# Kernel tuning notes

Measured on AMD Instinct MI355X. Metric: run time of the kernel, lower is better.

The kernel has to match this reference:

```python
import jax, jax.numpy as jnp
import numpy as np

N_INP = 1024
N_HID = 1024
N_OUT = 1024
B, S = 8, 2048


def setup_inputs() -> dict:
    key = jax.random.key(0)
    ks = jax.random.split(key, 9)
    s_in = 1.0 / np.sqrt(N_INP)
    s_hid = 1.0 / np.sqrt(N_HID)
    return {
        "x": jax.random.normal(ks[0], (B, S, N_INP), jnp.float32),
        "wq": jax.random.uniform(ks[1], (N_INP, N_HID), jnp.float32, -s_in, s_in),
        "bq": jax.random.uniform(ks[2], (N_HID,), jnp.float32, -s_in, s_in),
        "wk": jax.random.uniform(ks[3], (N_INP, N_HID), jnp.float32, -s_in, s_in),
        "bk": jax.random.uniform(ks[4], (N_HID,), jnp.float32, -s_in, s_in),
        "wv": jax.random.uniform(ks[5], (N_INP, N_HID), jnp.float32, -s_in, s_in),
        "bv": jax.random.uniform(ks[6], (N_HID,), jnp.float32, -s_in, s_in),
        "wo": jax.random.uniform(ks[7], (N_HID, N_OUT), jnp.float32, -s_hid, s_hid),
        "bo": jax.random.uniform(ks[8], (N_OUT,), jnp.float32, -s_hid, s_hid),
    }


def reference(x, wq, bq, wk, bk, wv, bv, wo, bo):
    # x: [B, S, n_inp]
    q = jnp.einsum("bsi,ih->bsh", x, wq) + bq  # [B,S,H]
    k = jnp.einsum("bsi,ih->bsh", x, wk) + bk
    v = jnp.einsum("bsi,ih->bsh", x, wv) + bv
    scale = 1.0 / jnp.sqrt(jnp.float32(N_HID))
    energy = jnp.einsum("bqh,bkh->bqk", q, k) * scale  # [B,S,S]
    attn = jax.nn.softmax(energy, axis=-1)  # dropout=0.0 (eval)
    ctx = jnp.einsum("bqk,bkh->bqh", attn, v)  # [B,S,H]
    out = jnp.einsum("bsh,ho->bso", ctx, wo) + bo  # [B,S,n_out]
    return out
```

## Files before the change

### kernel.cpp

```cpp
#include <hip/hip_runtime.h>
#include <hip/hip_bf16.h>


typedef __attribute__((ext_vector_type(8))) __bf16 bf16x8;
typedef __attribute__((ext_vector_type(4))) __bf16 bf16x4;
typedef __attribute__((ext_vector_type(4))) float  f32x4;
typedef __attribute__((ext_vector_type(8))) float  f32x8;

__device__ __forceinline__ void gl_lds16(const void* g, void* l) {
    __builtin_amdgcn_global_load_lds(
        (__attribute__((address_space(1))) const void*)g,
        (__attribute__((address_space(3))) void*)l, 16, 0, 0);
}

template <bool SWP>
__device__ __forceinline__ f32x4 mfma16(bf16x8 a, bf16x8 b, f32x4 c) {
    if constexpr (SWP)
        return __builtin_amdgcn_mfma_f32_16x16x32_bf16(b, a, c, 0, 0, 0);
    else
        return __builtin_amdgcn_mfma_f32_16x16x32_bf16(a, b, c, 0, 0, 0);
}

__global__ __launch_bounds__(256) void k_convert(const float* __restrict__ in,
                                                 __bf16* __restrict__ out) {
    const int i = blockIdx.x * 256 + threadIdx.x;
    f32x8 a = *((const f32x8*)in + i);
    bf16x8 o;
#pragma unroll
    for (int j = 0; j < 8; ++j) o[j] = (__bf16)a[j];
    *((bf16x8*)out + i) = o;
}

__global__ __launch_bounds__(256) void k_transpose_w(
    const float* __restrict__ w0, const float* __restrict__ w1,
    const float* __restrict__ w2, const float* __restrict__ w3,
    __bf16* __restrict__ Wt) {
    const int z = blockIdx.z;
    const float* W = (z == 0) ? w0 : (z == 1) ? w1 : (z == 2) ? w2 : w3;
    __bf16* Wo = Wt + (long long)z * 1048576;
    __shared__ float t[64][65];
    const int tid = threadIdx.x;
    const int c4 = (tid & 15) * 4, r0 = tid >> 4;
    const int bx = blockIdx.x * 64, by = blockIdx.y * 64;
#pragma unroll
    for (int p = 0; p < 4; ++p) {
        const int r = r0 + p * 16;
        f32x4 v = *(const f32x4*)(W + (long long)(by + r) * 1024 + bx + c4);
#pragma unroll
        for (int j = 0; j < 4; ++j) t[r][c4 + j] = v[j];
    }
    __syncthreads();
#pragma unroll
    for (int p = 0; p < 4; ++p) {
        const int r = r0 + p * 16;
        bf16x4 o;
#pragma unroll
        for (int j = 0; j < 4; ++j) o[j] = (__bf16)t[c4 + j][r];
        *(bf16x4*)(Wo + (long long)(bx + r) * 1024 + by + c4) = o;
    }
}

__global__ __launch_bounds__(256) void k_bcat(const float* __restrict__ bq,
                                              const float* __restrict__ bk,
                                              const float* __restrict__ bv,
                                              float* __restrict__ bc) {
    const int i = blockIdx.x * 256 + threadIdx.x;
    const float* s = (i < 1024) ? bq : (i < 2048 ? bk : bv);
    bc[i] = s[i & 1023];
}

__global__ __launch_bounds__(256) void k_softmax(__bf16* __restrict__ E) {
    __bf16* p = E + (long long)blockIdx.x * 2048;
    const int tid = threadIdx.x, l = tid & 63, w = tid >> 6;
    bf16x8 vb = *((const bf16x8*)p + tid);
    float v[8];
#pragma unroll
    for (int i = 0; i < 8; ++i) v[i] = (float)vb[i];
    float m = v[0];
#pragma unroll
    for (int i = 1; i < 8; ++i) m = fmaxf(m, v[i]);
    for (int off = 32; off > 0; off >>= 1) m = fmaxf(m, __shfl_xor(m, off));
    __shared__ float redm[4], reds[4];
    if (l == 0) redm[w] = m;
    __syncthreads();
    m = fmaxf(fmaxf(redm[0], redm[1]), fmaxf(redm[2], redm[3]));
    float e[8], s = 0.f;
#pragma unroll
    for (int i = 0; i < 8; ++i) { e[i] = __expf(v[i] - m); s += e[i]; }
    for (int off = 32; off > 0; off >>= 1) s += __shfl_xor(s, off);
    if (l == 0) reds[w] = s;
    __syncthreads();
    s = reds[0] + reds[1] + reds[2] + reds[3];
    const float inv = 1.0f / s;
    bf16x8 o;
#pragma unroll
    for (int i = 0; i < 8; ++i) o[i] = (__bf16)(e[i] * inv);
    *((bf16x8*)p + tid) = o;
}

template <int MODE, bool HAS_BIAS>
__global__ __launch_bounds__(512, 2) void gemm_bt(
    const __bf16* __restrict__ A, const __bf16* __restrict__ Bt,
    const float* __restrict__ bias, void* __restrict__ Cout,
    int K, int lda, int ldb, int ldc, int gy, int rpx, int bnc,
    float scale, long long sA, long long sB, long long sC) {
    constexpr bool SWP = (MODE != 4);
    __shared__ __align__(16) __bf16 Abuf0[16384];
    __shared__ __align__(16) __bf16 Bbuf0[16384];
    __shared__ __align__(16) __bf16 Abuf1[16384];
    __shared__ __align__(16) __bf16 Bbuf1[16384];

    const int lid = blockIdx.x;
    const int xcd = lid & 7;
    const int jj = lid >> 3;
    const int bn = jj % bnc;
    const int rt = xcd * rpx + jj / bnc;
    const int z = rt / gy;
    const int bm = rt - z * gy;

    const __bf16* Ab = A + (long long)z * sA;
    const __bf16* Bb = Bt + (long long)z * sB;

    const int tid = threadIdx.x;
    const int l = tid & 63, w = tid >> 6;
    const int wm = w >> 2, wn = w & 3;

    const int rA = tid >> 3;
    const int cswz = (tid & 7) ^ (rA & 7);
    const __bf16* aSg = Ab + (long long)(bm * 256 + rA) * lda + cswz * 8;
    const __bf16* bSg = Bb + (long long)(bn * 256 + rA) * ldb + cswz * 8;
    const long long a64 = (long long)lda * 64;
    const long long b64 = (long long)ldb * 64;
    const int ldst = tid * 16;

    const int r16 = l & 15, kq4 = l >> 4;
    const int sw0 = kq4 ^ (r16 & 7);
    const int aro0 = (wm * 128 + r16) * 64 + sw0 * 8;
    const int aro1 = aro0 ^ 32;
    const int bro0 = (wn * 64 + r16) * 64 + sw0 * 8;
    const int bro1 = bro0 ^ 32;

    f32x4 acc[8][4] = {};
    bf16x8 bf[4][2];

#define ST_A(buf, j, t)                                                    \
    gl_lds16(aSg + (j) * a64 + (long long)(t) * 64,                        \
             (char*)(buf) + ldst + (j) * 8192)
#define ST_B(buf, j, t)                                                    \
    gl_lds16(bSg + (j) * b64 + (long long)(t) * 64,                        \
             (char*)(buf) + ldst + (j) * 8192)

#define RD_B(buf)                                                          \
    do {                                                                   \
        _Pragma("unroll") for (int ni = 0; ni < 4; ++ni) {                 \
            bf[ni][0] = *(const bf16x8*)((buf) + bro0 + ni * 1024);        \
            bf[ni][1] = *(const bf16x8*)((buf) + bro1 + ni * 1024);        \
        }                                                                  \
    } while (0)

#define WV4 asm volatile("s_waitcnt vmcnt(4)" ::: "memory")
#define WV0 asm volatile("s_waitcnt vmcnt(0)" ::: "memory")
#define NOW ((void)0)

#define PHASE(Abuf, p, RB, RBUF, STAGES, WAIT)                                 \
    do {                                                                      \
        bf16x8 af0k0 = *(const bf16x8*)((Abuf) + aro0 + (2 * (p)) * 1024);     \
        bf16x8 af0k1 = *(const bf16x8*)((Abuf) + aro1 + (2 * (p)) * 1024);     \
        bf16x8 af1k0 = *(const bf16x8*)((Abuf) + aro0 + (2 * (p) + 1) * 1024); \
        bf16x8 af1k1 = *(const bf16x8*)((Abuf) + aro1 + (2 * (p) + 1) * 1024); \
        if (RB) RD_B(RBUF);                                                   \
        STAGES;                                                               \
        __builtin_amdgcn_s_barrier();                                         \
        asm volatile("s_waitcnt lgkmcnt(0)" ::: "memory");                    \
        __builtin_amdgcn_sched_barrier(0);                                    \
        __builtin_amdgcn_s_setprio(1);                                        \
        _Pragma("unroll") for (int ni = 0; ni < 4; ++ni) {                    \
            acc[2 * (p)][ni] = mfma16<SWP>(af0k0, bf[ni][0], acc[2*(p)][ni]); \
            acc[2 * (p)][ni] = mfma16<SWP>(af0k1, bf[ni][1], acc[2*(p)][ni]); \
            acc[2*(p)+1][ni] = mfma16<SWP>(af1k0, bf[ni][0], acc[2*(p)+1][ni]);\
            acc[2*(p)+1][ni] = mfma16<SWP>(af1k1, bf[ni][1], acc[2*(p)+1][ni]);\
        }                                                                     \
        __builtin_amdgcn_s_setprio(0);                                        \
        WAIT;                                                                 \
        __builtin_amdgcn_sched_barrier(0);                                    \
        __builtin_amdgcn_s_barrier();                                         \
    } while (0)

    ST_B(Bbuf0, 0, 0); ST_B(Bbuf0, 1, 0); ST_B(Bbuf0, 2, 0); ST_B(Bbuf0, 3, 0);
    ST_A(Abuf0, 0, 0); ST_A(Abuf0, 1, 0); ST_A(Abuf0, 2, 0); ST_A(Abuf0, 3, 0);
    ST_B(Bbuf1, 0, 1); ST_B(Bbuf1, 1, 1); ST_B(Bbuf1, 2, 1); ST_B(Bbuf1, 3, 1);
    WV4;
    __builtin_amdgcn_s_barrier();

    const int NT = K >> 6;
    for (int t0 = 0; t0 + 3 < NT; t0 += 2) {
        PHASE(Abuf0, 0, 1, Bbuf0,
              (ST_A(Abuf1, 0, t0 + 1), ST_A(Abuf1, 1, t0 + 1),
               ST_A(Abuf1, 2, t0 + 1), ST_A(Abuf1, 3, t0 + 1)), NOW);
        PHASE(Abuf0, 1, 0, Bbuf0,
              (ST_B(Bbuf0, 0, t0 + 2), ST_B(Bbuf0, 1, t0 + 2)), NOW);
        PHASE(Abuf0, 2, 0, Bbuf0,
              (ST_B(Bbuf0, 2, t0 + 2), ST_B(Bbuf0, 3, t0 + 2)), NOW);
        PHASE(Abuf0, 3, 0, Bbuf0, NOW, WV4);
        PHASE(Abuf1, 0, 1, Bbuf1,
              (ST_A(Abuf0, 0, t0 + 2), ST_A(Abuf0, 1, t0 + 2)), NOW);
        PHASE(Abuf1, 1, 0, Bbuf1,
              (ST_A(Abuf0, 2, t0 + 2), ST_A(Abuf0, 3, t0 + 2)), NOW);
        PHASE(Abuf1, 2, 0, Bbuf1,
              (ST_B(Bbuf1, 0, t0 + 3), ST_B(Bbuf1, 1, t0 + 3)), NOW);
        PHASE(Abuf1, 3, 0, Bbuf1,
              (ST_B(Bbuf1, 2, t0 + 3), ST_B(Bbuf1, 3, t0 + 3)), WV4);
    }
    {
        PHASE(Abuf0, 0, 1, Bbuf0,
              (ST_A(Abuf1, 0, NT - 1), ST_A(Abuf1, 1, NT - 1),
               ST_A(Abuf1, 2, NT - 1), ST_A(Abuf1, 3, NT - 1)), NOW);
        PHASE(Abuf0, 1, 0, Bbuf0, NOW, NOW);
        PHASE(Abuf0, 2, 0, Bbuf0, NOW, NOW);
        PHASE(Abuf0, 3, 0, Bbuf0, NOW, WV0);
        PHASE(Abuf1, 0, 1, Bbuf1, NOW, NOW);
        PHASE(Abuf1, 1, 0, Bbuf1, NOW, NOW);
        PHASE(Abuf1, 2, 0, Bbuf1, NOW, NOW);
        PHASE(Abuf1, 3, 0, Bbuf1, NOW, NOW);
    }
#undef ST_A
#undef ST_B
#undef RD_B
#undef WV4
#undef WV0
#undef NOW
#undef PHASE

    const int quad = kq4;
    if constexpr (MODE == 2) {
        __bf16* Qb = (__bf16*)Cout;
        const int part = bn >> 2;
#pragma unroll
        for (int mi = 0; mi < 8; ++mi) {
            const int srow0 = bm * 256 + wm * 128 + mi * 16 + r16;
            const int b = srow0 >> 11;
            const int s0 = srow0 & 2047;
#pragma unroll
            for (int ni = 0; ni < 4; ++ni) {
                const int col0 = bn * 256 + wn * 64 + ni * 16 + quad * 4;
                const f32x4 bb = *(const f32x4*)(bias + col0);
                const int c1 = col0 - part * 1024;
                bf16x4 o;
#pragma unroll
                for (int rr = 0; rr < 4; ++rr) o[rr] = (__bf16)(acc[mi][ni][rr] + bb[rr]);
                *(bf16x4*)(Qb + (long long)part * 16777216 +
                           (long long)b * 2097152 + (long long)s0 * 1024 + c1) = o;
            }
        }
    } else if constexpr (MODE == 4) {
        __bf16* Vb = (__bf16*)Cout;
#pragma unroll
        for (int mi = 0; mi < 8; ++mi) {
            const int srow0 = bm * 256 + wm * 128 + mi * 16 + quad * 4;
            const int b = srow0 >> 11;
            const int s0 = srow0 & 2047;
#pragma unroll
            for (int ni = 0; ni < 4; ++ni) {
                const int c1 = bn * 256 + wn * 64 + ni * 16 + r16;
                const float bb = HAS_BIAS ? bias[c1] : 0.0f;
                bf16x4 o;
#pragma unroll
                for (int rr = 0; rr < 4; ++rr) o[rr] = (__bf16)(acc[mi][ni][rr] + bb);
                *(bf16x4*)(Vb + (long long)b * 2097152 +
                           (long long)c1 * 2048 + s0) = o;
            }
        }
    } else {
        const long long cbase = (long long)z * sC;
#pragma unroll
        for (int mi = 0; mi < 8; ++mi) {
            const int row = bm * 256 + wm * 128 + mi * 16 + r16;
#pragma unroll
            for (int ni = 0; ni < 4; ++ni) {
                const int col0 = bn * 256 + wn * 64 + ni * 16 + quad * 4;
                f32x4 v;
                if constexpr (HAS_BIAS) {
                    const f32x4 bb = *(const f32x4*)(bias + col0);
#pragma unroll
                    for (int rr = 0; rr < 4; ++rr) v[rr] = acc[mi][ni][rr] * scale + bb[rr];
                } else {
#pragma unroll
                    for (int rr = 0; rr < 4; ++rr) v[rr] = acc[mi][ni][rr] * scale;
                }
                if constexpr (MODE == 1) {
                    *(f32x4*)((float*)Cout + cbase + (long long)row * ldc + col0) = v;
                } else {
                    bf16x4 o;
#pragma unroll
                    for (int rr = 0; rr < 4; ++rr) o[rr] = (__bf16)v[rr];
                    *(bf16x4*)((__bf16*)Cout + cbase + (long long)row * ldc + col0) = o;
                }
            }
        }
    }
}

extern "C" void kernel_launch(void* const* d_in, const int* in_sizes, int n_in,
                              void* d_out, int out_size, void* d_ws, size_t ws_size,
                              hipStream_t stream) {
    const float* x  = (const float*)d_in[0];
    const float* wq = (const float*)d_in[1];
    const float* bq = (const float*)d_in[2];
    const float* wk = (const float*)d_in[3];
    const float* bk = (const float*)d_in[4];
    const float* wv = (const float*)d_in[5];
    const float* bv = (const float*)d_in[6];
    const float* wo = (const float*)d_in[7];
    const float* bo = (const float*)d_in[8];
    float* out = (float*)d_out;

    __bf16* ws  = (__bf16*)d_ws;
    __bf16* Xb  = ws;
    __bf16* E   = ws;
    __bf16* Q   = ws + 33554432;
    __bf16* Kb  = ws + 50331648;
    __bf16* Vt  = ws + 67108864;
    __bf16* Ctx = ws + 83886080;
    __bf16* WT  = ws + 100663296;
    float*  bc  = (float*)(ws + 104857600);

    k_convert<<<8192, 256, 0, stream>>>(x, Xb);
    k_transpose_w<<<dim3(16, 16, 4), 256, 0, stream>>>(wq, wk, wv, wo, WT);
    k_bcat<<<12, 256, 0, stream>>>(bq, bk, bv, bc);

    gemm_bt<2, true><<<512, 512, 0, stream>>>(
        Xb, WT, bc, Q, 1024, 1024, 1024, 0, 64, 8, 8, 1.0f, 0, 0, 0);

    gemm_bt<4, true><<<256, 512, 0, stream>>>(
        Xb, WT + 2097152, bc + 2048, Vt, 1024, 1024, 1024, 0, 64, 8, 4,
        1.0f, 0, 0, 0);

    gemm_bt<0, false><<<512, 512, 0, stream>>>(
        Q, Kb, nullptr, E, 1024, 1024, 1024, 2048, 8, 8, 8,
        0.03125f, 2097152, 2097152, 4194304);

    k_softmax<<<16384, 256, 0, stream>>>(E);

    gemm_bt<0, false><<<256, 512, 0, stream>>>(
        E, Vt, nullptr, Ctx, 2048, 2048, 2048, 1024, 8, 8, 4,
        1.0f, 4194304, 2097152, 2097152);

    gemm_bt<1, true><<<256, 512, 0, stream>>>(
        Ctx, WT + 3145728, bo, out, 1024, 1024, 1024, 1024, 64, 8, 4,
        1.0f, 0, 0, 0);
}
```

Before: 446.8 us.

## Software-pipeline LDS fragment reads ahead of MFMAs with double-buffered registers

Restructures the GEMM main loop so that the A and B fragments for the next phase are read from LDS into a second register set while the current phase's MFMAs run. Partial lgkmcnt waits replace the full drain, and each phase now has one barrier instead of two. The global-to-LDS stage schedule is reordered, with the Abuf1 prefetch moved into the prologue. This hides LDS read latency behind matrix math, at the cost of more registers, which may lower occupancy. The waitcnt counting is subtle and could cause races if any count is wrong.

```diff
diff --git a/kernel.cpp b/kernel.cpp
--- a/kernel.cpp
+++ b/kernel.cpp
@@ -141,7 +141,9 @@
     const int bro1 = bro0 ^ 32;
 
     f32x4 acc[8][4] = {};
-    bf16x8 bf[4][2];
+    bf16x8 bfX[4][2], bfY[4][2];
+    bf16x8 sAk00, sAk01, sAk10, sAk11;
+    bf16x8 tAk00, tAk01, tAk10, tAk11;
 
 #define ST_A(buf, j, t)                                                    \
     gl_lds16(aSg + (j) * a64 + (long long)(t) * 64,                        \
@@ -150,86 +152,101 @@
     gl_lds16(bSg + (j) * b64 + (long long)(t) * 64,                        \
              (char*)(buf) + ldst + (j) * 8192)
 
-#define RD_B(buf)                                                          \
+#define PRA(N, buf, np)                                                    \
+    do {                                                                   \
+        N##k00 = *(const bf16x8*)((buf) + aro0 + (2 * (np)) * 1024);       \
+        N##k01 = *(const bf16x8*)((buf) + aro1 + (2 * (np)) * 1024);       \
+        N##k10 = *(const bf16x8*)((buf) + aro0 + (2 * (np) + 1) * 1024);   \
+        N##k11 = *(const bf16x8*)((buf) + aro1 + (2 * (np) + 1) * 1024);   \
+    } while (0)
+
+#define PRB(BN, buf)                                                       \
     do {                                                                   \
         _Pragma("unroll") for (int ni = 0; ni < 4; ++ni) {                 \
-            bf[ni][0] = *(const bf16x8*)((buf) + bro0 + ni * 1024);        \
-            bf[ni][1] = *(const bf16x8*)((buf) + bro1 + ni * 1024);        \
+            BN[ni][0] = *(const bf16x8*)((buf) + bro0 + ni * 1024);        \
+            BN[ni][1] = *(const bf16x8*)((buf) + bro1 + ni * 1024);        \
         }                                                                  \
     } while (0)
 
-#define WV4 asm volatile("s_waitcnt vmcnt(4)" ::: "memory")
-#define WV0 asm volatile("s_waitcnt vmcnt(0)" ::: "memory")
-#define NOW ((void)0)
-
-#define PHASE(Abuf, p, RB, RBUF, STAGES, WAIT)                                 \
+#define MM16(pp, U, BC)                                                       \
     do {                                                                      \
-        bf16x8 af0k0 = *(const bf16x8*)((Abuf) + aro0 + (2 * (p)) * 1024);     \
-        bf16x8 af0k1 = *(const bf16x8*)((Abuf) + aro1 + (2 * (p)) * 1024);     \
-        bf16x8 af1k0 = *(const bf16x8*)((Abuf) + aro0 + (2 * (p) + 1) * 1024); \
-        bf16x8 af1k1 = *(const bf16x8*)((Abuf) + aro1 + (2 * (p) + 1) * 1024); \
-        if (RB) RD_B(RBUF);                                                   \
-        STAGES;                                                               \
-        __builtin_amdgcn_s_barrier();                                         \
-        asm volatile("s_waitcnt lgkmcnt(0)" ::: "memory");                    \
-        __builtin_amdgcn_sched_barrier(0);                                    \
         __builtin_amdgcn_s_setprio(1);                                        \
         _Pragma("unroll") for (int ni = 0; ni < 4; ++ni) {                    \
-            acc[2 * (p)][ni] = mfma16<SWP>(af0k0, bf[ni][0], acc[2*(p)][ni]); \
-            acc[2 * (p)][ni] = mfma16<SWP>(af0k1, bf[ni][1], acc[2*(p)][ni]); \
-            acc[2*(p)+1][ni] = mfma16<SWP>(af1k0, bf[ni][0], acc[2*(p)+1][ni]);\
-            acc[2*(p)+1][ni] = mfma16<SWP>(af1k1, bf[ni][1], acc[2*(p)+1][ni]);\
+            acc[2*(pp)][ni]   = mfma16<SWP>(U##k00, BC[ni][0], acc[2*(pp)][ni]);   \
+            acc[2*(pp)+1][ni] = mfma16<SWP>(U##k10, BC[ni][0], acc[2*(pp)+1][ni]); \
+        }                                                                     \
+        _Pragma("unroll") for (int ni = 0; ni < 4; ++ni) {                    \
+            acc[2*(pp)][ni]   = mfma16<SWP>(U##k01, BC[ni][1], acc[2*(pp)][ni]);   \
+            acc[2*(pp)+1][ni] = mfma16<SWP>(U##k11, BC[ni][1], acc[2*(pp)+1][ni]); \
         }                                                                     \
         __builtin_amdgcn_s_setprio(0);                                        \
-        WAIT;                                                                 \
-        __builtin_amdgcn_sched_barrier(0);                                    \
-        __builtin_amdgcn_s_barrier();                                         \
+    } while (0)
+
+#define LGK(n)                                                             \
+    do {                                                                   \
+        asm volatile("s_waitcnt lgkmcnt(" #n ")" ::: "memory");            \
+        __builtin_amdgcn_sched_barrier(0);                                 \
+    } while (0)
+#define WVC(n) asm volatile("s_waitcnt vmcnt(" #n ")" ::: "memory")
+#define BARR                                                               \
+    do {                                                                   \
+        __builtin_amdgcn_s_barrier();                                      \
+        __builtin_amdgcn_sched_barrier(0);                                 \
     } while (0)
 
     ST_B(Bbuf0, 0, 0); ST_B(Bbuf0, 1, 0); ST_B(Bbuf0, 2, 0); ST_B(Bbuf0, 3, 0);
     ST_A(Abuf0, 0, 0); ST_A(Abuf0, 1, 0); ST_A(Abuf0, 2, 0); ST_A(Abuf0, 3, 0);
     ST_B(Bbuf1, 0, 1); ST_B(Bbuf1, 1, 1); ST_B(Bbuf1, 2, 1); ST_B(Bbuf1, 3, 1);
-    WV4;
-    __builtin_amdgcn_s_barrier();
+    ST_A(Abuf1, 0, 1); ST_A(Abuf1, 1, 1); ST_A(Abuf1, 2, 1); ST_A(Abuf1, 3, 1);
+    WVC(8);
+    BARR;
+    PRB(bfX, Bbuf0);
+    PRA(sA, Abuf0, 0);
 
     const int NT = K >> 6;
     for (int t0 = 0; t0 + 3 < NT; t0 += 2) {
-        PHASE(Abuf0, 0, 1, Bbuf0,
-              (ST_A(Abuf1, 0, t0 + 1), ST_A(Abuf1, 1, t0 + 1),
-               ST_A(Abuf1, 2, t0 + 1), ST_A(Abuf1, 3, t0 + 1)), NOW);
-        PHASE(Abuf0, 1, 0, Bbuf0,
-              (ST_B(Bbuf0, 0, t0 + 2), ST_B(Bbuf0, 1, t0 + 2)), NOW);
-        PHASE(Abuf0, 2, 0, Bbuf0,
-              (ST_B(Bbuf0, 2, t0 + 2), ST_B(Bbuf0, 3, t0 + 2)), NOW);
-        PHASE(Abuf0, 3, 0, Bbuf0, NOW, WV4);
-        PHASE(Abuf1, 0, 1, Bbuf1,
-              (ST_A(Abuf0, 0, t0 + 2), ST_A(Abuf0, 1, t0 + 2)), NOW);
-        PHASE(Abuf1, 1, 0, Bbuf1,
-              (ST_A(Abuf0, 2, t0 + 2), ST_A(Abuf0, 3, t0 + 2)), NOW);
-        PHASE(Abuf1, 2, 0, Bbuf1,
-              (ST_B(Bbuf1, 0, t0 + 3), ST_B(Bbuf1, 1, t0 + 3)), NOW);
-        PHASE(Abuf1, 3, 0, Bbuf1,
-              (ST_B(Bbuf1, 2, t0 + 3), ST_B(Bbuf1, 3, t0 + 3)), WV4);
+        ST_B(Bbuf0, 0, t0 + 2); ST_B(Bbuf0, 1, t0 + 2);
+        PRA(tA, Abuf0, 1);
+        LGK(4); MM16(0, sA, bfX); BARR;
+        ST_B(Bbuf0, 2, t0 + 2); ST_B(Bbuf0, 3, t0 + 2);
+        PRA(sA, Abuf0, 2);
+        LGK(4); MM16(1, tA, bfX); BARR;
+        PRA(tA, Abuf0, 3);
+        LGK(4); MM16(2, sA, bfX); WVC(4); BARR;
+        ST_A(Abuf0, 0, t0 + 2); ST_A(Abuf0, 1, t0 + 2);
+        PRB(bfY, Bbuf1); PRA(sA, Abuf1, 0);
+        LGK(12); MM16(3, tA, bfX); BARR;
+        ST_A(Abuf0, 2, t0 + 2); ST_A(Abuf0, 3, t0 + 2);
+        PRA(tA, Abuf1, 1);
+        LGK(4); MM16(0, sA, bfY); BARR;
+        ST_B(Bbuf1, 0, t0 + 3); ST_B(Bbuf1, 1, t0 + 3);
+        PRA(sA, Abuf1, 2);
+        LGK(4); MM16(1, tA, bfY); BARR;
+        ST_B(Bbuf1, 2, t0 + 3); ST_B(Bbuf1, 3, t0 + 3);
+        PRA(tA, Abuf1, 3);
+        LGK(4); MM16(2, sA, bfY); WVC(4); BARR;
+        ST_A(Abuf1, 0, t0 + 3); ST_A(Abuf1, 1, t0 + 3);
+        ST_A(Abuf1, 2, t0 + 3); ST_A(Abuf1, 3, t0 + 3);
+        PRB(bfX, Bbuf0); PRA(sA, Abuf0, 0);
+        LGK(12); MM16(3, tA, bfY); BARR;
     }
-    {
-        PHASE(Abuf0, 0, 1, Bbuf0,
-              (ST_A(Abuf1, 0, NT - 1), ST_A(Abuf1, 1, NT - 1),
-               ST_A(Abuf1, 2, NT - 1), ST_A(Abuf1, 3, NT - 1)), NOW);
-        PHASE(Abuf0, 1, 0, Bbuf0, NOW, NOW);
-        PHASE(Abuf0, 2, 0, Bbuf0, NOW, NOW);
-        PHASE(Abuf0, 3, 0, Bbuf0, NOW, WV0);
-        PHASE(Abuf1, 0, 1, Bbuf1, NOW, NOW);
-        PHASE(Abuf1, 1, 0, Bbuf1, NOW, NOW);
-        PHASE(Abuf1, 2, 0, Bbuf1, NOW, NOW);
-        PHASE(Abuf1, 3, 0, Bbuf1, NOW, NOW);
-    }
+    PRA(tA, Abuf0, 1); LGK(4);  MM16(0, sA, bfX); BARR;
+    PRA(sA, Abuf0, 2); LGK(4);  MM16(1, tA, bfX); BARR;
+    PRA(tA, Abuf0, 3); LGK(4);  MM16(2, sA, bfX); WVC(0); BARR;
+    PRB(bfY, Bbuf1); PRA(sA, Abuf1, 0);
+    LGK(12); MM16(3, tA, bfX); BARR;
+    PRA(tA, Abuf1, 1); LGK(4);  MM16(0, sA, bfY); BARR;
+    PRA(sA, Abuf1, 2); LGK(4);  MM16(1, tA, bfY); BARR;
+    PRA(tA, Abuf1, 3); LGK(4);  MM16(2, sA, bfY); BARR;
+    LGK(0); MM16(3, tA, bfY);
 #undef ST_A
 #undef ST_B
-#undef RD_B
-#undef WV4
-#undef WV0
-#undef NOW
-#undef PHASE
+#undef PRA
+#undef PRB
+#undef MM16
+#undef LGK
+#undef WVC
+#undef BARR
 
     const int quad = kq4;
     if constexpr (MODE == 2) {
```

Result: slower. 669.3 us (+49.8%).
